# Kernel optimization log

Hardware: AMD Instinct MI355X
Metric: run time of the kernel (lower is better)

The kernel has to match this reference:

```python
import jax, jax.numpy as jnp
import numpy as np

H = 1024            # hinges
S = 4               # shims
N = H + 2           # nodes
NC = 2 * N          # flattened DOFs
B = 256             # batch of independent chains
L = 1.0             # rest edge length
DT = 0.001          # integration step
GAMMA = 2.0         # damping
N_STEPS = 64        # relaxation steps (truncated scan)


def setup_inputs() -> dict:
    key = jax.random.key(0)
    k1, k2, k3, k4, k5 = jax.random.split(key, 5)
    xs = jnp.arange(N, dtype=jnp.float32) * L
    base = jnp.stack([xs, jnp.zeros(N, jnp.float32)], axis=-1)          # (N,2) straight chain
    noise = 0.01 * jax.random.normal(k1, (B, N, 2), jnp.float32)
    noise = noise.at[:, :2, :].set(0.0)                                  # nodes 0,1 fixed exactly
    pos0 = base[None] + noise                                            # (B,N,2)
    tip_base = base[-1]
    tip_off = jnp.stack([-0.1 * L * H * jax.random.uniform(k2, (B,)),
                         2.0 * jax.random.normal(k3, (B,))], axis=-1)
    tip_pos = (tip_base[None] + tip_off).astype(jnp.float32)             # (B,2) imposed tip
    thetas_ss = 0.3 * jax.random.uniform(k4, (H,), jnp.float32)          # snap-through angles
    buckle_arr = jax.random.randint(k5, (H, S), 0, 2).astype(jnp.int32)  # {0,1} -> maps to {-1,+1}
    return dict(pos0=pos0, tip_pos=tip_pos, thetas_ss=thetas_ss, buckle_arr=buckle_arr,
                k_stiff=jnp.float32(10.0), k_soft=jnp.float32(0.5), k_stretch=jnp.float32(1000.0))


def _free_mask():
    m = np.ones(NC, bool)
    m[:4] = False            # nodes 0,1 fixed (dof_idx = 2*node+comp)
    m[2 * (N - 1):] = False  # tip node imposed
    return jnp.asarray(m)


def _energy(x, thetas_ss, buckle_pm, k_stiff, k_soft, k_stretch):
    """Total potential energy of one chain; x is flattened (NC,)."""
    pos = x.reshape(N, 2)
    v1 = pos[1:-1] - pos[:-2]                 # (H,2) edge into hinge h
    v2 = pos[2:] - pos[1:-1]                  # (H,2) edge out of hinge h
    theta = jnp.arctan2(v1[:, 0] * v2[:, 1] - v1[:, 1] * v2[:, 0],
                        jnp.sum(v1 * v2, -1))               # (H,) CCW hinge angle
    d = pos[1:] - pos[:-1]
    elen = jnp.sqrt(jnp.sum(d * d, -1))                     # (H+1,) edge lengths
    T = theta[:, None]                                      # (H,1)
    TH = thetas_ss[:, None]                                 # (H,1)
    stiff = ((buckle_pm == 1) & (T < TH)) | ((buckle_pm == -1) & (T > -TH))  # (H,S)
    k_rot = jnp.where(stiff, k_stiff, k_soft)
    e_rot = 0.5 * jnp.sum(k_rot * (T - TH) ** 2)
    e_str = 0.5 * jnp.sum(k_stretch * (elen - L) ** 2)
    return e_rot + e_str


def reference(pos0, tip_pos, thetas_ss, buckle_arr, k_stiff, k_soft, k_stretch):
    buckle_pm = 2 * buckle_arr - 1                           # {0,1} -> {-1,+1}
    free = _free_mask()                                      # (NC,) static
    x0 = pos0.reshape(B, NC)
    x0 = x0.at[:, 2 * (N - 1)].set(tip_pos[:, 0]).at[:, 2 * (N - 1) + 1].set(tip_pos[:, 1])
    v0 = jnp.zeros_like(x0)

    grad_e = jax.vmap(jax.grad(
        lambda x: _energy(x, thetas_ss, buckle_pm, k_stiff, k_soft, k_stretch)))

    def step(carry, _):
        x, v = carry
        f = -grad_e(x)                                       # potential force, (B,NC)
        v = jnp.where(free[None], v + DT * (f - GAMMA * v), 0.0)
        x = jnp.where(free[None], x + DT * v, x)             # fixed/imposed DOFs held
        return (x, v), None

    (xf, _vf), _ = jax.lax.scan(step, (x0, v0), None, length=N_STEPS)
    return xf                                                # (B,NC) relaxed positions
```

## Files before the change

kernel.cpp:

```cpp
#include <hip/hip_runtime.h>

#define NN 1026
#define NE 1025
#define NA 1024
#define BLK 1024

__device__ __forceinline__ float fast_atan2f(float y, float x) {
    float ax = __builtin_fabsf(x), ay = __builtin_fabsf(y);
    float mx = fmaxf(ax, ay), mn = fminf(ax, ay);
    float a  = mn * __builtin_amdgcn_rcpf(mx);
    float s  = a * a;
    float r  = fmaf(s, -0.0117212f,  0.05265332f);
    r = fmaf(s, r, -0.11643287f);
    r = fmaf(s, r,  0.19354346f);
    r = fmaf(s, r, -0.33262347f);
    r = fmaf(s, r,  0.99997726f);
    r *= a;
    if (ay > ax)  r = 1.57079637f - r;
    if (x < 0.0f) r = 3.14159274f - r;
    return copysignf(r, y);
}

__global__ __launch_bounds__(BLK)
void equil_kernel(const float* __restrict__ pos0,
                  const float* __restrict__ tip_pos,
                  const float* __restrict__ thetas_ss,
                  const int*   __restrict__ buckle,
                  const float* __restrict__ kstiff_p,
                  const float* __restrict__ ksoft_p,
                  const float* __restrict__ kstretch_p,
                  float* __restrict__ out)
{
    __shared__ float2 pos[NN];
    __shared__ float2 Ps[NE];
    __shared__ float2 Qs[NA];
    __shared__ float2 Bs[NA];

    const int b   = blockIdx.x;
    const int tid = threadIdx.x;
    const float k_str  = kstretch_p[0];
    const float k_sd   = kstiff_p[0] - ksoft_p[0];
    const float k4soft = 4.0f * ksoft_p[0];

    const float2* p0 = (const float2*)(pos0 + (size_t)b * NN * 2);
    pos[tid] = p0[tid];
    if (tid == 0) pos[NA] = p0[NA];
    if (tid == 1) {
        float2 t; t.x = tip_pos[2*b]; t.y = tip_pos[2*b+1];
        pos[NN-1] = t;
    }
    const float TH = thetas_ss[tid];
    const int4 bk  = ((const int4*)buckle)[tid];
    const float npl = (float)(bk.x + bk.y + bk.z + bk.w);
    float vxr = 0.f, vyr = 0.f;
    __syncthreads();
    float2 myp = pos[tid + 2];

    for (int s = 0; s < 64; ++s) {
        float2 pa = pos[tid], pb = pos[tid+1], pc = pos[tid+2];
        float v1x = pb.x - pa.x, v1y = pb.y - pa.y;
        float v2x = pc.x - pb.x, v2y = pc.y - pb.y;
        float l2a = fmaf(v1x, v1x, v1y * v1y);
        float l2b = fmaf(v2x, v2x, v2y * v2y);
        float cr  = v1x * v2y - v1y * v2x;
        float dt_ = fmaf(v1x, v2x, v1y * v2y);
        float theta = fast_atan2f(cr, dt_);
        float cnt = (theta <  TH ? npl        : 0.f)
                  + (theta > -TH ? 4.f - npl  : 0.f);
        float K = fmaf(cnt, k_sd, k4soft);
        float m = K * (theta - TH);
        float ila = __builtin_amdgcn_rsqf(l2a);
        float ilb = __builtin_amdgcn_rsqf(l2b);
        float m1 = m * ila * ila;
        float m2 = m * ilb * ilb;
        float2 av; av.x =  m1 * v1y;  av.y = -m1 * v1x;
        float2 bv; bv.x = -m2 * v2y;  bv.y =  m2 * v2x;
        float sca = k_str * (1.0f - ila);
        float2 P;  P.x = fmaf(sca, v1x, av.x);  P.y = fmaf(sca, v1y, av.y);
        float2 Q;  Q.x = P.x - bv.x;            Q.y = P.y - bv.y;
        Ps[tid] = P;
        Qs[tid] = Q;
        Bs[tid] = bv;
        if (tid == NA - 1) {
            float scb = k_str * (1.0f - ilb);
            float2 PN; PN.x = scb * v2x; PN.y = scb * v2y;
            Ps[NA] = PN;
        }
        __syncthreads();

        if (tid <= NN - 4) {
            const int i = tid + 2;
            float2 Pn = Ps[i];
            float2 Qm = Qs[i-1];
            float2 Bm = Bs[i-2];
            float fx = Pn.x - Qm.x - Bm.x;
            float fy = Pn.y - Qm.y - Bm.y;
            vxr += 0.001f * (fx - 2.0f * vxr);
            vyr += 0.001f * (fy - 2.0f * vyr);
            myp.x += 0.001f * vxr;
            myp.y += 0.001f * vyr;
            pos[i] = myp;
        }
        __syncthreads();
    }

    float2* o = (float2*)(out + (size_t)b * NN * 2);
    o[tid] = pos[tid];
    if (tid < 2) o[NA + tid] = pos[NA + tid];
}

extern "C" void kernel_launch(void* const* d_in, const int* in_sizes, int n_in,
                              void* d_out, int out_size, void* d_ws, size_t ws_size,
                              hipStream_t stream) {
    const float* pos0   = (const float*)d_in[0];
    const float* tip    = (const float*)d_in[1];
    const float* thetas = (const float*)d_in[2];
    const int*   buckle = (const int*)  d_in[3];
    const float* ks     = (const float*)d_in[4];
    const float* ko     = (const float*)d_in[5];
    const float* kr     = (const float*)d_in[6];
    float* out = (float*)d_out;
    hipLaunchKernelGGL(equil_kernel, dim3(256), dim3(BLK), 0, stream,
                       pos0, tip, thetas, buckle, ks, ko, kr, out);
}
```

Baseline: 49.07 us.

## Replace shared-memory neighbor exchange with wavefront shuffles plus halo buffers

Neighbour positions and the per-hinge force terms (P, Q, B) are now exchanged with wavefront shuffles inside each 64-lane wave. Only the two boundary lanes of each wave go through small shared halo arrays. Each thread keeps its own node position in registers instead of a shared pos array. This cuts LDS traffic and bank pressure per step. It adds shuffle instructions and branchy boundary handling, and the two block barriers per step remain.

```diff
diff --git a/kernel.cpp b/kernel.cpp
--- a/kernel.cpp
+++ b/kernel.cpp
@@ -1,8 +1,5 @@
 #include <hip/hip_runtime.h>
 
-#define NN 1026
-#define NE 1025
-#define NA 1024
 #define BLK 1024
 
 __device__ __forceinline__ float fast_atan2f(float y, float x) {
@@ -31,35 +28,43 @@
                   const float* __restrict__ kstretch_p,
                   float* __restrict__ out)
 {
-    __shared__ float2 pos[NN];
-    __shared__ float2 Ps[NE];
-    __shared__ float2 Qs[NA];
-    __shared__ float2 Bs[NA];
+    __shared__ float2 bM[16][2];
+    __shared__ float2 bP[17][2];
+    __shared__ float2 bQ[17];
 
-    const int b   = blockIdx.x;
-    const int tid = threadIdx.x;
+    const int b  = blockIdx.x;
+    const int t  = threadIdx.x;
+    const int wv = t >> 6, ln = t & 63;
     const float k_str  = kstretch_p[0];
     const float k_sd   = kstiff_p[0] - ksoft_p[0];
     const float k4soft = 4.0f * ksoft_p[0];
 
-    const float2* p0 = (const float2*)(pos0 + (size_t)b * NN * 2);
-    pos[tid] = p0[tid];
-    if (tid == 0) pos[NA] = p0[NA];
-    if (tid == 1) {
-        float2 t; t.x = tip_pos[2*b]; t.y = tip_pos[2*b+1];
-        pos[NN-1] = t;
-    }
-    const float TH = thetas_ss[tid];
-    const int4 bk  = ((const int4*)buckle)[tid];
+    const float2* p0 = (const float2*)(pos0 + (size_t)b * 2052);
+    const float2 c0 = p0[0], c1 = p0[1];
+    float2 tip; tip.x = tip_pos[2*b]; tip.y = tip_pos[2*b+1];
+
+    float2 myp = (t < 1023) ? p0[t + 2] : tip;
+
+    const float TH = thetas_ss[t];
+    const int4 bk  = ((const int4*)buckle)[t];
     const float npl = (float)(bk.x + bk.y + bk.z + bk.w);
-    float vxr = 0.f, vyr = 0.f;
+    float2 vel = make_float2(0.f, 0.f);
+
+    if (ln >= 62) bM[wv][ln - 62] = myp;
     __syncthreads();
-    float2 myp = pos[tid + 2];
 
     for (int s = 0; s < 64; ++s) {
-        float2 pa = pos[tid], pb = pos[tid+1], pc = pos[tid+2];
-        float v1x = pb.x - pa.x, v1y = pb.y - pa.y;
-        float v2x = pc.x - pb.x, v2y = pc.y - pb.y;
+        float2 pm1, pm2;
+        pm1.x = __shfl_up(myp.x, 1, 64);  pm1.y = __shfl_up(myp.y, 1, 64);
+        pm2.x = __shfl_up(myp.x, 2, 64);  pm2.y = __shfl_up(myp.y, 2, 64);
+        if (ln == 0) {
+            pm1 = wv ? bM[wv-1][1] : c1;
+            pm2 = wv ? bM[wv-1][0] : c0;
+        } else if (ln == 1) {
+            pm2 = wv ? bM[wv-1][1] : c1;
+        }
+        float v1x = pm1.x - pm2.x, v1y = pm1.y - pm2.y;
+        float v2x = myp.x - pm1.x, v2y = myp.y - pm1.y;
         float l2a = fmaf(v1x, v1x, v1y * v1y);
         float l2b = fmaf(v2x, v2x, v2y * v2y);
         float cr  = v1x * v2y - v1y * v2x;
@@ -73,40 +78,41 @@
         float ilb = __builtin_amdgcn_rsqf(l2b);
         float m1 = m * ila * ila;
         float m2 = m * ilb * ilb;
-        float2 av; av.x =  m1 * v1y;  av.y = -m1 * v1x;
-        float2 bv; bv.x = -m2 * v2y;  bv.y =  m2 * v2x;
+        float2 Bv; Bv.x = -m2 * v2y;  Bv.y =  m2 * v2x;
         float sca = k_str * (1.0f - ila);
-        float2 P;  P.x = fmaf(sca, v1x, av.x);  P.y = fmaf(sca, v1y, av.y);
-        float2 Q;  Q.x = P.x - bv.x;            Q.y = P.y - bv.y;
-        Ps[tid] = P;
-        Qs[tid] = Q;
-        Bs[tid] = bv;
-        if (tid == NA - 1) {
+        float2 P;  P.x = fmaf(sca, v1x,  m1 * v1y);
+        P.y = fmaf(sca, v1y, -m1 * v1x);
+        float2 Q;  Q.x = P.x - Bv.x;  Q.y = P.y - Bv.y;
+        if (ln == 0)      { bP[wv][0] = P; bQ[wv] = Q; }
+        else if (ln == 1) { bP[wv][1] = P; }
+        if (t == 1023) {
             float scb = k_str * (1.0f - ilb);
             float2 PN; PN.x = scb * v2x; PN.y = scb * v2y;
-            Ps[NA] = PN;
+            bP[16][0] = PN;
         }
         __syncthreads();
 
-        if (tid <= NN - 4) {
-            const int i = tid + 2;
-            float2 Pn = Ps[i];
-            float2 Qm = Qs[i-1];
-            float2 Bm = Bs[i-2];
-            float fx = Pn.x - Qm.x - Bm.x;
-            float fy = Pn.y - Qm.y - Bm.y;
-            vxr += 0.001f * (fx - 2.0f * vxr);
-            vyr += 0.001f * (fy - 2.0f * vyr);
-            myp.x += 0.001f * vxr;
-            myp.y += 0.001f * vyr;
-            pos[i] = myp;
+        float2 Pn, Qm;
+        Pn.x = __shfl_down(P.x, 2, 64);  Pn.y = __shfl_down(P.y, 2, 64);
+        Qm.x = __shfl_down(Q.x, 1, 64);  Qm.y = __shfl_down(Q.y, 1, 64);
+        if (ln == 62)      { Pn = bP[wv+1][0]; }
+        else if (ln == 63) { Pn = bP[wv+1][1]; Qm = bQ[wv+1]; }
+        if (t < 1023) {
+            float fx = Pn.x - Qm.x - Bv.x;
+            float fy = Pn.y - Qm.y - Bv.y;
+            vel.x += 0.001f * (fx - 2.0f * vel.x);
+            vel.y += 0.001f * (fy - 2.0f * vel.y);
+            myp.x += 0.001f * vel.x;
+            myp.y += 0.001f * vel.y;
         }
+        if (ln >= 62) bM[wv][ln - 62] = myp;
         __syncthreads();
     }
 
-    float2* o = (float2*)(out + (size_t)b * NN * 2);
-    o[tid] = pos[tid];
-    if (tid < 2) o[NA + tid] = pos[NA + tid];
+    float2* o = (float2*)(out + (size_t)b * 2052);
+    o[t + 2] = myp;
+    if (t == 0) o[0] = c0;
+    if (t == 1) o[1] = c1;
 }
 
 extern "C" void kernel_launch(void* const* d_in, const int* in_sizes, int n_in,
```

New measurement: 65.99 us. +34.5%, slower.
